# Kernel optimization log

Measured on AMD Instinct MI355X. Metric: run time of the kernel, lower is better.

Reference implementation:

```python
import jax, jax.numpy as jnp
import numpy as np

D_MODEL = 512
NHEAD = 4
HEAD_DIM = D_MODEL // NHEAD


def setup_inputs() -> dict:
    key = jax.random.key(0)
    ks = jax.random.split(key, 12)
    B, S = 2, 4096
    s = 1.0 / np.sqrt(D_MODEL)
    inp = {
        "query": jax.random.normal(ks[0], (B, S, D_MODEL), jnp.float32),
        "key": jax.random.normal(ks[1], (B, S, D_MODEL), jnp.float32),
        "value": jax.random.normal(ks[2], (B, S, D_MODEL), jnp.float32),
        "Wq": jax.random.uniform(ks[3], (D_MODEL, D_MODEL), jnp.float32, -s, s),
        "bq": jax.random.uniform(ks[4], (D_MODEL,), jnp.float32, -s, s),
        "Wk": jax.random.uniform(ks[5], (D_MODEL, D_MODEL), jnp.float32, -s, s),
        "bk": jax.random.uniform(ks[6], (D_MODEL,), jnp.float32, -s, s),
        "Wv": jax.random.uniform(ks[7], (D_MODEL, D_MODEL), jnp.float32, -s, s),
        "bv": jax.random.uniform(ks[8], (D_MODEL,), jnp.float32, -s, s),
        "Wo": jax.random.uniform(ks[9], (D_MODEL, D_MODEL), jnp.float32, -s, s),
        "bo": jax.random.uniform(ks[10], (D_MODEL,), jnp.float32, -s, s),
    }
    return inp


def reference(query, key, value, Wq, bq, Wk, bk, Wv, bv, Wo, bo):
    B, Sq, _ = query.shape
    Sk = key.shape[1]
    # projections (torch Linear: x @ W.T + b); split heads -> [B, H, S, hd]
    def proj(x, W, b, S):
        return (x @ W.T + b).reshape(B, S, NHEAD, HEAD_DIM).transpose(0, 2, 1, 3)
    Q = proj(query, Wq, bq, Sq)
    K = proj(key, Wk, bk, Sk)
    V = proj(value, Wv, bv, Sk)
    scale = 1.0 / np.sqrt(HEAD_DIM).astype(np.float32)
    scores = jnp.einsum("bhqd,bhkd->bhqk", Q, K) * scale  # [B,H,Sq,Sk]
    weights = jax.nn.softmax(scores, axis=-1)
    out = jnp.einsum("bhqk,bhkd->bhqd", weights, V)  # [B,H,Sq,hd]
    out = out.transpose(0, 2, 1, 3).reshape(B, Sq, D_MODEL)
    return out @ Wo.T + bo
```

## Files before the change

kernel.cpp:

```cpp
#include <hip/hip_runtime.h>


#define D_MODEL 512
#define NHEAD 4
#define HD 128
#define S_ 4096

typedef __attribute__((ext_vector_type(8))) short bf16x8;
typedef __attribute__((ext_vector_type(4))) short bf16x4;
typedef __attribute__((ext_vector_type(4))) float f32x4;
typedef __attribute__((ext_vector_type(2))) unsigned uint2v;
typedef __attribute__((ext_vector_type(4))) unsigned uint4v;

#define SCQ (0.08838834764831845f * 1.4426950408889634f)

__device__ __forceinline__ short f2bf(float f) {
    unsigned u = __builtin_bit_cast(unsigned, f);
    u += 0x7fffu + ((u >> 16) & 1u);
    return (short)(u >> 16);
}
__device__ __forceinline__ unsigned pk2bf(float a, float b) {
    unsigned ua = __builtin_bit_cast(unsigned, a);
    ua += 0x7fffu + ((ua >> 16) & 1u);
    unsigned ub = __builtin_bit_cast(unsigned, b);
    ub += 0x7fffu + ((ub >> 16) & 1u);
    return (ua >> 16) | (ub & 0xffff0000u);
}
__device__ __forceinline__ void gl2lds16(const short* g, short* l) {
    __builtin_amdgcn_global_load_lds(
        (const __attribute__((address_space(1))) void*)g,
        (__attribute__((address_space(3))) void*)l, 16, 0, 0);
}

__global__ __launch_bounds__(256) void convert_kernel(
    const float* __restrict__ s0, const float* __restrict__ s1,
    const float* __restrict__ s2, const float* __restrict__ s3,
    const float* __restrict__ s4, const float* __restrict__ s5,
    const float* __restrict__ s6,
    short* __restrict__ d0, short* __restrict__ d1, short* __restrict__ d2,
    short* __restrict__ d3, short* __restrict__ d4, short* __restrict__ d5,
    short* __restrict__ d6)
{
    int seg = blockIdx.y;
    const float* src; short* dst; int n;
    const int NBIG = 2 * S_ * D_MODEL;
    const int NW = D_MODEL * D_MODEL;
    switch (seg) {
        case 0: src = s0; dst = d0; n = NBIG; break;
        case 1: src = s1; dst = d1; n = NBIG; break;
        case 2: src = s2; dst = d2; n = NBIG; break;
        case 3: src = s3; dst = d3; n = NW; break;
        case 4: src = s4; dst = d4; n = NW; break;
        case 5: src = s5; dst = d5; n = NW; break;
        default: src = s6; dst = d6; n = NW; break;
    }
    int idx = (blockIdx.x * 256 + threadIdx.x) * 8;
    if (idx >= n) return;
    float4 a = *(const float4*)(src + idx);
    float4 b = *(const float4*)(src + idx + 4);
    uint4v o;
    o[0] = pk2bf(a.x, a.y); o[1] = pk2bf(a.z, a.w);
    o[2] = pk2bf(b.x, b.y); o[3] = pk2bf(b.z, b.w);
    *(uint4v*)(dst + idx) = o;
}

__global__ __launch_bounds__(256) void qkv_kernel(
    const short* __restrict__ qb, const short* __restrict__ kb,
    const short* __restrict__ vb,
    const short* __restrict__ Wqb, const short* __restrict__ Wkb,
    const short* __restrict__ Wvb,
    const float* __restrict__ bq, const float* __restrict__ bk,
    const float* __restrict__ bv,
    short* __restrict__ Qh, short* __restrict__ Kh, short* __restrict__ VT)
{
    __shared__ short smem[24576];
    int z = blockIdx.z;
    const short* A    = (z == 0) ? qb  : (z == 1) ? kb  : vb;
    const short* W    = (z == 0) ? Wqb : (z == 1) ? Wkb : Wvb;
    const float* bias = (z == 0) ? bq  : (z == 1) ? bk  : bv;
    short* out        = (z == 0) ? Qh  : (z == 1) ? Kh  : VT;
    int vmode = (z == 2);
    float osc = (z == 0) ? SCQ : 1.0f;

    int t = threadIdx.x;
    int wv = t >> 6, ln = t & 63, q4 = ln >> 4, c = ln & 15;
    int m0 = blockIdx.x * 64, n0 = blockIdx.y * 128;
    f32x4 acc[8] = {};

    {
        short* lAd = smem;
        short* lBd = smem + 8192;
        #pragma unroll
        for (int i = 0; i < 2; ++i) {
            int id = i * 256 + t;
            int m = id >> 3, kgp = id & 7;
            gl2lds16(A + (size_t)(m0 + m) * 512 + ((kgp ^ (m & 7)) << 3), &lAd[id * 8]);
        }
        #pragma unroll
        for (int i = 0; i < 4; ++i) {
            int id = i * 256 + t;
            int n = id >> 3, kgp = id & 7;
            gl2lds16(W + (size_t)(n0 + n) * 512 + ((kgp ^ (n & 7)) << 3), &lBd[id * 8]);
        }
    }
    asm volatile("s_waitcnt vmcnt(0)" ::: "memory");
    __builtin_amdgcn_s_barrier();
    __builtin_amdgcn_sched_barrier(0);

    int cur = 0;
    for (int k0 = 0; k0 < 512; k0 += 64) {
        int more = (k0 < 448);
        if (more) {
            short* lAd = smem + (cur ^ 1) * 4096;
            short* lBd = smem + 8192 + (cur ^ 1) * 8192;
            int kn = k0 + 64;
            #pragma unroll
            for (int i = 0; i < 2; ++i) {
                int id = i * 256 + t;
                int m = id >> 3, kgp = id & 7;
                gl2lds16(A + (size_t)(m0 + m) * 512 + kn + ((kgp ^ (m & 7)) << 3), &lAd[id * 8]);
            }
            #pragma unroll
            for (int i = 0; i < 4; ++i) {
                int id = i * 256 + t;
                int n = id >> 3, kgp = id & 7;
                gl2lds16(W + (size_t)(n0 + n) * 512 + kn + ((kgp ^ (n & 7)) << 3), &lBd[id * 8]);
            }
        }
        short* lAc = smem + cur * 4096;
        short* lBc = smem + 8192 + cur * 8192;
        __builtin_amdgcn_s_setprio(1);
        #pragma unroll
        for (int ks = 0; ks < 2; ++ks) {
            int kg = ks * 4 + q4;
            int m = wv * 16 + c;
            bf16x8 af = *(bf16x8*)&lAc[m * 64 + ((kg ^ (m & 7)) << 3)];
            bf16x8 bfr[8];
            #pragma unroll
            for (int nt = 0; nt < 8; ++nt) {
                int n = nt * 16 + c;
                bfr[nt] = *(bf16x8*)&lBc[n * 64 + ((kg ^ (n & 7)) << 3)];
            }
            #pragma unroll
            for (int nt = 0; nt < 8; ++nt)
                acc[nt] = __builtin_amdgcn_mfma_f32_16x16x32_bf16(af, bfr[nt], acc[nt], 0, 0, 0);
        }
        __builtin_amdgcn_s_setprio(0);
        if (more) asm volatile("s_waitcnt vmcnt(0)" ::: "memory");
        __builtin_amdgcn_s_barrier();
        __builtin_amdgcn_sched_barrier(0);
        cur ^= 1;
    }

    if (vmode == 0) {
        const int TS = 136;
        short* lT = smem;
        for (int nt = 0; nt < 8; ++nt) {
            float bv_ = bias[n0 + nt * 16 + c];
            for (int r = 0; r < 4; ++r) {
                int srow = wv * 16 + q4 * 4 + r;
                lT[srow * TS + nt * 16 + c] = f2bf((acc[nt][r] + bv_) * osc);
            }
        }
        __syncthreads();
        int bb = m0 >> 12, sbase = m0 & 4095, h = blockIdx.y;
        for (int i = 0; i < 4; ++i) {
            int id = i * 256 + t;
            int row = id >> 4, g = id & 15;
            bf16x8 vv = *(bf16x8*)&lT[row * TS + g * 8];
            *(bf16x8*)&out[((size_t)((bb * NHEAD + h) * S_ + sbase + row)) * HD + g * 8] = vv;
        }
    } else {
        short* lB0 = smem + 8192;
        for (int nt = 0; nt < 8; ++nt) {
            int d = nt * 16 + c;
            float bv_ = bias[n0 + d];
            uint2v pv;
            pv[0] = pk2bf(acc[nt][0] + bv_, acc[nt][1] + bv_);
            pv[1] = pk2bf(acc[nt][2] + bv_, acc[nt][3] + bv_);
            int gr = wv * 4 + q4;
            *(uint2v*)&lB0[d * 64 + ((gr ^ (d & 15)) << 2)] = pv;
        }
        __syncthreads();
        int bb = m0 >> 12, sbase = m0 & 4095, h = blockIdx.y;
        for (int i = 0; i < 8; ++i) {
            int id = i * 256 + t;
            int d = id >> 4, grl = id & 15;
            bf16x4 v = *(bf16x4*)&lB0[d * 64 + ((grl ^ (d & 15)) << 2)];
            *(bf16x4*)&out[((size_t)((bb * NHEAD + h) * HD + d)) * S_ + sbase + grl * 4] = v;
        }
    }
}

__global__ __launch_bounds__(256) void outproj_kernel(
    const short* __restrict__ A, const short* __restrict__ W,
    const float* __restrict__ bias, float* __restrict__ out)
{
    __shared__ short smem[24576];
    int t = threadIdx.x;
    int wv = t >> 6, ln = t & 63, q4 = ln >> 4, c = ln & 15;
    int m0 = blockIdx.x * 64, n0 = blockIdx.y * 128;
    f32x4 acc[8] = {};

    {
        short* lAd = smem;
        short* lBd = smem + 8192;
        #pragma unroll
        for (int i = 0; i < 2; ++i) {
            int id = i * 256 + t;
            int m = id >> 3, kgp = id & 7;
            gl2lds16(A + (size_t)(m0 + m) * 512 + ((kgp ^ (m & 7)) << 3), &lAd[id * 8]);
        }
        #pragma unroll
        for (int i = 0; i < 4; ++i) {
            int id = i * 256 + t;
            int n = id >> 3, kgp = id & 7;
            gl2lds16(W + (size_t)(n0 + n) * 512 + ((kgp ^ (n & 7)) << 3), &lBd[id * 8]);
        }
    }
    asm volatile("s_waitcnt vmcnt(0)" ::: "memory");
    __builtin_amdgcn_s_barrier();
    __builtin_amdgcn_sched_barrier(0);

    int cur = 0;
    for (int k0 = 0; k0 < 512; k0 += 64) {
        int more = (k0 < 448);
        if (more) {
            short* lAd = smem + (cur ^ 1) * 4096;
            short* lBd = smem + 8192 + (cur ^ 1) * 8192;
            int kn = k0 + 64;
            #pragma unroll
            for (int i = 0; i < 2; ++i) {
                int id = i * 256 + t;
                int m = id >> 3, kgp = id & 7;
                gl2lds16(A + (size_t)(m0 + m) * 512 + kn + ((kgp ^ (m & 7)) << 3), &lAd[id * 8]);
            }
            #pragma unroll
            for (int i = 0; i < 4; ++i) {
                int id = i * 256 + t;
                int n = id >> 3, kgp = id & 7;
                gl2lds16(W + (size_t)(n0 + n) * 512 + kn + ((kgp ^ (n & 7)) << 3), &lBd[id * 8]);
            }
        }
        short* lAc = smem + cur * 4096;
        short* lBc = smem + 8192 + cur * 8192;
        __builtin_amdgcn_s_setprio(1);
        #pragma unroll
        for (int ks = 0; ks < 2; ++ks) {
            int kg = ks * 4 + q4;
            int m = wv * 16 + c;
            bf16x8 af = *(bf16x8*)&lAc[m * 64 + ((kg ^ (m & 7)) << 3)];
            bf16x8 bfr[8];
            #pragma unroll
            for (int nt = 0; nt < 8; ++nt) {
                int n = nt * 16 + c;
                bfr[nt] = *(bf16x8*)&lBc[n * 64 + ((kg ^ (n & 7)) << 3)];
            }
            #pragma unroll
            for (int nt = 0; nt < 8; ++nt)
                acc[nt] = __builtin_amdgcn_mfma_f32_16x16x32_bf16(af, bfr[nt], acc[nt], 0, 0, 0);
        }
        __builtin_amdgcn_s_setprio(0);
        if (more) asm volatile("s_waitcnt vmcnt(0)" ::: "memory");
        __builtin_amdgcn_s_barrier();
        __builtin_amdgcn_sched_barrier(0);
        cur ^= 1;
    }

    for (int nt = 0; nt < 8; ++nt) {
        int col = n0 + nt * 16 + c;
        float bv_ = bias[col];
        for (int r = 0; r < 4; ++r) {
            int mrow = m0 + wv * 16 + q4 * 4 + r;
            out[(size_t)mrow * 512 + col] = acc[nt][r] + bv_;
        }
    }
}

__global__ __launch_bounds__(256, 2) void flash_kernel(
    const short* __restrict__ Qh, const short* __restrict__ Kh,
    const short* __restrict__ VTg, short* __restrict__ AO,
    float* __restrict__ U, float* __restrict__ ML, int nsplit, int kkspan)
{
    __shared__ short lK[2][64 * 128];
    __shared__ short lVT[128 * 64];
    int t = threadIdx.x;
    int wv = t >> 6, ln = t & 63, q4 = ln >> 4, c = ln & 15;
    int bh = blockIdx.x;
    int s0 = blockIdx.y * 128;
    int z = blockIdx.z;
    const size_t base = (size_t)bh * S_ * HD;

    bf16x8 qf[2][4];
    #pragma unroll
    for (int qt = 0; qt < 2; ++qt) {
        int s = s0 + wv * 32 + qt * 16 + c;
        const short* qp = Qh + base + (size_t)s * HD + q4 * 8;
        #pragma unroll
        for (int ks = 0; ks < 4; ++ks)
            qf[qt][ks] = *(const bf16x8*)(qp + ks * 32);
    }

    f32x4 of[8][2] = {};
    float lrun[2] = {};

    int kkbeg = z * kkspan;
    int nt = kkspan >> 6;

    #pragma unroll
    for (int i = 0; i < 4; ++i) {
        int id = i * 256 + t;
        int m = id >> 4, kgp = id & 15;
        gl2lds16(Kh + base + (size_t)(kkbeg + m) * HD + ((kgp ^ (m & 7)) << 3),
                 &lK[0][id * 8]);
    }
    #pragma unroll
    for (int i = 0; i < 4; ++i) {
        int id = i * 256 + t;
        int mv = id >> 3, kgvp = id & 7;
        gl2lds16(VTg + base + (size_t)mv * S_ + kkbeg + ((kgvp ^ (mv & 7)) << 3),
                 &lVT[id * 8]);
    }
    asm volatile("s_waitcnt vmcnt(4)" ::: "memory");
    __builtin_amdgcn_s_barrier();
    __builtin_amdgcn_sched_barrier(0);

    int cur = 0;
    for (int it = 0; it < nt; ++it) {
        int kk0 = kkbeg + it * 64;
        int more = (it + 1 < nt);

        if (more) {
            #pragma unroll
            for (int i = 0; i < 4; ++i) {
                int id = i * 256 + t;
                int m = id >> 4, kgp = id & 15;
                gl2lds16(Kh + base + (size_t)(kk0 + 64 + m) * HD + ((kgp ^ (m & 7)) << 3),
                         &lK[cur ^ 1][id * 8]);
            }
        }

        f32x4 sf[2][4] = {};
        __builtin_amdgcn_s_setprio(1);
        #pragma unroll
        for (int ks = 0; ks < 4; ++ks) {
            int kg = ks * 4 + q4;
            bf16x8 af[4];
            #pragma unroll
            for (int kt = 0; kt < 4; ++kt) {
                int row = kt * 16 + c;
                af[kt] = *(bf16x8*)&lK[cur][row * 128 + ((kg ^ (row & 7)) << 3)];
            }
            #pragma unroll
            for (int qt = 0; qt < 2; ++qt)
                #pragma unroll
                for (int kt = 0; kt < 4; ++kt)
                    sf[qt][kt] = __builtin_amdgcn_mfma_f32_16x16x32_bf16(
                        af[kt], qf[qt][ks], sf[qt][kt], 0, 0, 0);
        }
        __builtin_amdgcn_s_setprio(0);

        bf16x8 bp[2][2];
        #pragma unroll
        for (int qt = 0; qt < 2; ++qt) {
            unsigned dlo[4], dhi[4];
            float lt = 0.f;
            #pragma unroll
            for (int kt = 0; kt < 4; ++kt) {
                float p0 = exp2f(sf[qt][kt][0]);
                float p1 = exp2f(sf[qt][kt][1]);
                float p2 = exp2f(sf[qt][kt][2]);
                float p3 = exp2f(sf[qt][kt][3]);
                lt += (p0 + p1) + (p2 + p3);
                asm("v_cvt_pk_bf16_f32 %0, %1, %2" : "=v"(dlo[kt]) : "v"(p0), "v"(p1));
                asm("v_cvt_pk_bf16_f32 %0, %1, %2" : "=v"(dhi[kt]) : "v"(p2), "v"(p3));
            }
            lrun[qt] += lt;
            #pragma unroll
            for (int ksv = 0; ksv < 2; ++ksv) {
                unsigned x0 = dlo[2 * ksv], y0 = dlo[2 * ksv + 1];
                unsigned x1 = dhi[2 * ksv], y1 = dhi[2 * ksv + 1];
                asm("v_permlane32_swap_b32 %0, %1" : "+v"(x0), "+v"(y0));
                asm("v_permlane16_swap_b32 %0, %1" : "+v"(x0), "+v"(y0));
                asm("v_permlane32_swap_b32 %0, %1" : "+v"(x1), "+v"(y1));
                asm("v_permlane16_swap_b32 %0, %1" : "+v"(x1), "+v"(y1));
                uint4v u; u[0] = x0; u[1] = x1; u[2] = y0; u[3] = y1;
                bp[qt][ksv] = __builtin_bit_cast(bf16x8, u);
            }
        }

        if (more) asm volatile("s_waitcnt vmcnt(4)" ::: "memory");
        else      asm volatile("s_waitcnt vmcnt(0)" ::: "memory");
        __builtin_amdgcn_s_barrier();
        __builtin_amdgcn_sched_barrier(0);

        __builtin_amdgcn_s_setprio(1);
        #pragma unroll
        for (int ksv = 0; ksv < 2; ++ksv) {
            int kg = ksv * 4 + q4;
            bf16x8 av[8];
            #pragma unroll
            for (int dt = 0; dt < 8; ++dt) {
                int row = dt * 16 + c;
                av[dt] = *(bf16x8*)&lVT[row * 64 + ((kg ^ (row & 7)) << 3)];
            }
            #pragma unroll
            for (int qt = 0; qt < 2; ++qt)
                #pragma unroll
                for (int dt = 0; dt < 8; ++dt)
                    of[dt][qt] = __builtin_amdgcn_mfma_f32_16x16x32_bf16(
                        av[dt], bp[qt][ksv], of[dt][qt], 0, 0, 0);
        }
        __builtin_amdgcn_s_setprio(0);

        asm volatile("s_waitcnt vmcnt(0)" ::: "memory");
        __builtin_amdgcn_s_barrier();
        __builtin_amdgcn_sched_barrier(0);

        if (more) {
            #pragma unroll
            for (int i = 0; i < 4; ++i) {
                int id = i * 256 + t;
                int mv = id >> 3, kgvp = id & 7;
                gl2lds16(VTg + base + (size_t)mv * S_ + kk0 + 64 + ((kgvp ^ (mv & 7)) << 3),
                         &lVT[id * 8]);
            }
        }
        cur ^= 1;
    }

    #pragma unroll
    for (int qt = 0; qt < 2; ++qt) {
        lrun[qt] += __shfl_xor(lrun[qt], 16);
        lrun[qt] += __shfl_xor(lrun[qt], 32);
    }

    if (nsplit > 1) {
        #pragma unroll
        for (int qt = 0; qt < 2; ++qt) {
            int s = s0 + wv * 32 + qt * 16 + c;
            size_t rowu = (size_t)(z * 8 + bh) * S_ + s;
            float* up = U + rowu * HD;
            #pragma unroll
            for (int dt = 0; dt < 8; ++dt)
                *(f32x4*)&up[dt * 16 + q4 * 4] = of[dt][qt];
            if (q4 == 0) ML[rowu] = lrun[qt];
        }
    } else {
        int b = bh >> 2, h = bh & 3;
        #pragma unroll
        for (int qt = 0; qt < 2; ++qt) {
            float inv = 1.0f / lrun[qt];
            int s = s0 + wv * 32 + qt * 16 + c;
            short* dst = AO + ((size_t)(b * S_ + s)) * D_MODEL + h * HD;
            #pragma unroll
            for (int dt = 0; dt < 8; ++dt) {
                uint2v ov;
                ov[0] = pk2bf(of[dt][qt][0] * inv, of[dt][qt][1] * inv);
                ov[1] = pk2bf(of[dt][qt][2] * inv, of[dt][qt][3] * inv);
                *(uint2v*)(dst + dt * 16 + q4 * 4) = ov;
            }
        }
    }
}

__global__ __launch_bounds__(256) void combine_kernel(
    const float* __restrict__ U, const float* __restrict__ ML,
    short* __restrict__ AO, int nsplit)
{
    int row = blockIdx.x * 8 + (threadIdx.x >> 5);
    int d4 = (threadIdx.x & 31) * 4;
    const int R = 8 * S_;
    float l = 0.f;
    f32x4 u = {0.f, 0.f, 0.f, 0.f};
    for (int zz = 0; zz < nsplit; ++zz) {
        l += ML[(size_t)zz * R + row];
        f32x4 uz = *(const f32x4*)&U[((size_t)zz * R + row) * HD + d4];
        u += uz;
    }
    float inv = 1.0f / l;
    uint2v o;
    o[0] = pk2bf(u[0] * inv, u[1] * inv);
    o[1] = pk2bf(u[2] * inv, u[3] * inv);
    int bh = row >> 12, s = row & 4095;
    int b = bh >> 2, h = bh & 3;
    *(uint2v*)&AO[((size_t)(b * S_ + s)) * D_MODEL + h * HD + d4] = o;
}

extern "C" void kernel_launch(void* const* d_in, const int* in_sizes, int n_in,
                              void* d_out, int out_size, void* d_ws, size_t ws_size,
                              hipStream_t stream) {
    const float* q  = (const float*)d_in[0];
    const float* k  = (const float*)d_in[1];
    const float* v  = (const float*)d_in[2];
    const float* Wq = (const float*)d_in[3];
    const float* bq = (const float*)d_in[4];
    const float* Wk = (const float*)d_in[5];
    const float* bk = (const float*)d_in[6];
    const float* Wv = (const float*)d_in[7];
    const float* bv = (const float*)d_in[8];
    const float* Wo = (const float*)d_in[9];
    const float* bo = (const float*)d_in[10];

    const size_t HS = (size_t)2 * NHEAD * S_ * HD;
    const size_t NBIG = HS;
    const size_t NW = (size_t)D_MODEL * D_MODEL;
    const size_t R = (size_t)8 * S_;

    char* wsb = (char*)d_ws;
    short* Qh = (short*)wsb;
    short* Kh = Qh + HS;
    short* VT = Kh + HS;
    short* AO = VT + HS;
    char* r2 = wsb + 4 * HS * 2;
    short* qb  = (short*)r2;
    short* kb  = qb + NBIG;
    short* vb  = kb + NBIG;
    short* Wqb = vb + NBIG;
    short* Wkb = Wqb + NW;
    short* Wvb = Wkb + NW;
    float* U   = (float*)r2;

    int nsplit = 1;
    size_t r2sz = 3 * NBIG * 2 + 3 * NW * 2;
    {
        int cand = 2;
        size_t r2c = (size_t)cand * R * HD * 4;
        if (r2c < 3 * NBIG * 2 + 3 * NW * 2) r2c = 3 * NBIG * 2 + 3 * NW * 2;
        size_t need = 4 * HS * 2 + r2c + (size_t)cand * R * 4 + NW * 2;
        if (ws_size >= need) { nsplit = cand; r2sz = r2c; }
    }
    float* ML  = (float*)(r2 + r2sz);
    short* Wob = (short*)((char*)ML + (size_t)nsplit * R * 4);
    int kkspan = S_ / nsplit;

    dim3 blk(256);
    convert_kernel<<<dim3(2048, 7), blk, 0, stream>>>(
        q, k, v, Wq, Wk, Wv, Wo, qb, kb, vb, Wqb, Wkb, Wvb, Wob);
    qkv_kernel<<<dim3(128, 4, 3), blk, 0, stream>>>(
        qb, kb, vb, Wqb, Wkb, Wvb, bq, bk, bv, Qh, Kh, VT);
    flash_kernel<<<dim3(8, 32, nsplit), blk, 0, stream>>>(
        Qh, Kh, VT, AO, U, ML, nsplit, kkspan);
    if (nsplit > 1)
        combine_kernel<<<dim3(S_), blk, 0, stream>>>(U, ML, AO, nsplit);
    outproj_kernel<<<dim3(128, 4), blk, 0, stream>>>(AO, Wob, bo, (float*)d_out);
}
```

Measured before the change: 228.4 us.

## Software-pipeline flash loop: overlap QK of next tile with PV of previous

```diff
diff --git a/kernel.cpp b/kernel.cpp
--- a/kernel.cpp
+++ b/kernel.cpp
@@ -277,13 +277,105 @@
     }
 }
 
+__device__ __forceinline__ void stage_k(const short* __restrict__ Kh, size_t base,
+                                        int kk, short* dst, int t) {
+    #pragma unroll
+    for (int i = 0; i < 4; ++i) {
+        int id = i * 256 + t;
+        int m = id >> 4, kgp = id & 15;
+        gl2lds16(Kh + base + (size_t)(kk + m) * HD + ((kgp ^ (m & 7)) << 3), &dst[id * 8]);
+    }
+}
+__device__ __forceinline__ void stage_vt(const short* __restrict__ VTg, size_t base,
+                                         int kk, short* dst, int t) {
+    #pragma unroll
+    for (int i = 0; i < 4; ++i) {
+        int id = i * 256 + t;
+        int mv = id >> 3, kgvp = id & 7;
+        gl2lds16(VTg + base + (size_t)mv * S_ + kk + ((kgvp ^ (mv & 7)) << 3), &dst[id * 8]);
+    }
+}
+__device__ __forceinline__ void qk_tile(const short* kb, const bf16x8 (&qf)[2][4],
+                                        int q4, int c, f32x4 (&sf)[2][4]) {
+    #pragma unroll
+    for (int ks = 0; ks < 4; ++ks) {
+        int kg = ks * 4 + q4;
+        bf16x8 af[4];
+        #pragma unroll
+        for (int kt = 0; kt < 4; ++kt) {
+            int row = kt * 16 + c;
+            af[kt] = *(bf16x8*)&kb[row * 128 + ((kg ^ (row & 7)) << 3)];
+        }
+        #pragma unroll
+        for (int qt = 0; qt < 2; ++qt)
+            #pragma unroll
+            for (int kt = 0; kt < 4; ++kt)
+                sf[qt][kt] = __builtin_amdgcn_mfma_f32_16x16x32_bf16(
+                    af[kt], qf[qt][ks], sf[qt][kt], 0, 0, 0);
+    }
+}
+__device__ __forceinline__ void pv_tile(const short* vb, const bf16x8 (&bp)[2][2],
+                                        int q4, int c, f32x4 (&of)[8][2]) {
+    #pragma unroll
+    for (int ksv = 0; ksv < 2; ++ksv) {
+        int kg = ksv * 4 + q4;
+        bf16x8 av[8];
+        #pragma unroll
+        for (int dt = 0; dt < 8; ++dt) {
+            int row = dt * 16 + c;
+            av[dt] = *(bf16x8*)&vb[row * 64 + ((kg ^ (row & 7)) << 3)];
+        }
+        #pragma unroll
+        for (int qt = 0; qt < 2; ++qt)
+            #pragma unroll
+            for (int dt = 0; dt < 8; ++dt)
+                of[dt][qt] = __builtin_amdgcn_mfma_f32_16x16x32_bf16(
+                    av[dt], bp[qt][ksv], of[dt][qt], 0, 0, 0);
+    }
+}
+__device__ __forceinline__ void sm_tile(const f32x4 (&sf)[2][4], float (&lrun)[2],
+                                        bf16x8 (&bp)[2][2]) {
+    #pragma unroll
+    for (int qt = 0; qt < 2; ++qt) {
+        unsigned dlo[4], dhi[4];
+        float lt = 0.f;
+        #pragma unroll
+        for (int kt = 0; kt < 4; ++kt) {
+            float p0 = exp2f(sf[qt][kt][0]);
+            float p1 = exp2f(sf[qt][kt][1]);
+            float p2 = exp2f(sf[qt][kt][2]);
+            float p3 = exp2f(sf[qt][kt][3]);
+            lt += (p0 + p1) + (p2 + p3);
+            asm("v_cvt_pk_bf16_f32 %0, %1, %2" : "=v"(dlo[kt]) : "v"(p0), "v"(p1));
+            asm("v_cvt_pk_bf16_f32 %0, %1, %2" : "=v"(dhi[kt]) : "v"(p2), "v"(p3));
+        }
+        lrun[qt] += lt;
+        #pragma unroll
+        for (int ksv = 0; ksv < 2; ++ksv) {
+            unsigned x0 = dlo[2 * ksv], y0 = dlo[2 * ksv + 1];
+            unsigned x1 = dhi[2 * ksv], y1 = dhi[2 * ksv + 1];
+            asm("v_permlane32_swap_b32 %0, %1" : "+v"(x0), "+v"(y0));
+            asm("v_permlane16_swap_b32 %0, %1" : "+v"(x0), "+v"(y0));
+            asm("v_permlane32_swap_b32 %0, %1" : "+v"(x1), "+v"(y1));
+            asm("v_permlane16_swap_b32 %0, %1" : "+v"(x1), "+v"(y1));
+            uint4v u; u[0] = x0; u[1] = x1; u[2] = y0; u[3] = y1;
+            bp[qt][ksv] = __builtin_bit_cast(bf16x8, u);
+        }
+    }
+}
+
+#define FLASH_BAR() do { \
+    asm volatile("s_waitcnt vmcnt(0)" ::: "memory"); \
+    __builtin_amdgcn_s_barrier(); \
+    __builtin_amdgcn_sched_barrier(0); } while (0)
+
 __global__ __launch_bounds__(256, 2) void flash_kernel(
     const short* __restrict__ Qh, const short* __restrict__ Kh,
     const short* __restrict__ VTg, short* __restrict__ AO,
     float* __restrict__ U, float* __restrict__ ML, int nsplit, int kkspan)
 {
     __shared__ short lK[2][64 * 128];
-    __shared__ short lVT[128 * 64];
+    __shared__ short lVT[2][128 * 64];
     int t = threadIdx.x;
     int wv = t >> 6, ln = t & 63, q4 = ln >> 4, c = ln & 15;
     int bh = blockIdx.x;
@@ -303,131 +395,67 @@
 
     f32x4 of[8][2] = {};
     float lrun[2] = {};
+    bf16x8 bpA[2][2], bpB[2][2];
 
     int kkbeg = z * kkspan;
-    int nt = kkspan >> 6;
-
-    #pragma unroll
-    for (int i = 0; i < 4; ++i) {
-        int id = i * 256 + t;
-        int m = id >> 4, kgp = id & 15;
-        gl2lds16(Kh + base + (size_t)(kkbeg + m) * HD + ((kgp ^ (m & 7)) << 3),
-                 &lK[0][id * 8]);
-    }
-    #pragma unroll
-    for (int i = 0; i < 4; ++i) {
-        int id = i * 256 + t;
-        int mv = id >> 3, kgvp = id & 7;
-        gl2lds16(VTg + base + (size_t)mv * S_ + kkbeg + ((kgvp ^ (mv & 7)) << 3),
-                 &lVT[id * 8]);
-    }
-    asm volatile("s_waitcnt vmcnt(4)" ::: "memory");
-    __builtin_amdgcn_s_barrier();
-    __builtin_amdgcn_sched_barrier(0);
-
-    int cur = 0;
-    for (int it = 0; it < nt; ++it) {
-        int kk0 = kkbeg + it * 64;
-        int more = (it + 1 < nt);
-
-        if (more) {
-            #pragma unroll
-            for (int i = 0; i < 4; ++i) {
-                int id = i * 256 + t;
-                int m = id >> 4, kgp = id & 15;
-                gl2lds16(Kh + base + (size_t)(kk0 + 64 + m) * HD + ((kgp ^ (m & 7)) << 3),
-                         &lK[cur ^ 1][id * 8]);
-            }
-        }
-
+    int ntl = kkspan >> 6;
+
+    stage_k(Kh, base, kkbeg, &lK[0][0], t);
+    FLASH_BAR();
+
+    {
+        stage_k(Kh, base, kkbeg + 64, &lK[1][0], t);
+        stage_vt(VTg, base, kkbeg, &lVT[0][0], t);
         f32x4 sf[2][4] = {};
         __builtin_amdgcn_s_setprio(1);
-        #pragma unroll
-        for (int ks = 0; ks < 4; ++ks) {
-            int kg = ks * 4 + q4;
-            bf16x8 af[4];
-            #pragma unroll
-            for (int kt = 0; kt < 4; ++kt) {
-                int row = kt * 16 + c;
-                af[kt] = *(bf16x8*)&lK[cur][row * 128 + ((kg ^ (row & 7)) << 3)];
-            }
-            #pragma unroll
-            for (int qt = 0; qt < 2; ++qt)
-                #pragma unroll
-                for (int kt = 0; kt < 4; ++kt)
-                    sf[qt][kt] = __builtin_amdgcn_mfma_f32_16x16x32_bf16(
-                        af[kt], qf[qt][ks], sf[qt][kt], 0, 0, 0);
-        }
+        qk_tile(&lK[0][0], qf, q4, c, sf);
         __builtin_amdgcn_s_setprio(0);
-
-        bf16x8 bp[2][2];
-        #pragma unroll
-        for (int qt = 0; qt < 2; ++qt) {
-            unsigned dlo[4], dhi[4];
-            float lt = 0.f;
-            #pragma unroll
-            for (int kt = 0; kt < 4; ++kt) {
-                float p0 = exp2f(sf[qt][kt][0]);
-                float p1 = exp2f(sf[qt][kt][1]);
-                float p2 = exp2f(sf[qt][kt][2]);
-                float p3 = exp2f(sf[qt][kt][3]);
-                lt += (p0 + p1) + (p2 + p3);
-                asm("v_cvt_pk_bf16_f32 %0, %1, %2" : "=v"(dlo[kt]) : "v"(p0), "v"(p1));
-                asm("v_cvt_pk_bf16_f32 %0, %1, %2" : "=v"(dhi[kt]) : "v"(p2), "v"(p3));
-            }
-            lrun[qt] += lt;
-            #pragma unroll
-            for (int ksv = 0; ksv < 2; ++ksv) {
-                unsigned x0 = dlo[2 * ksv], y0 = dlo[2 * ksv + 1];
-                unsigned x1 = dhi[2 * ksv], y1 = dhi[2 * ksv + 1];
-                asm("v_permlane32_swap_b32 %0, %1" : "+v"(x0), "+v"(y0));
-                asm("v_permlane16_swap_b32 %0, %1" : "+v"(x0), "+v"(y0));
-                asm("v_permlane32_swap_b32 %0, %1" : "+v"(x1), "+v"(y1));
-                asm("v_permlane16_swap_b32 %0, %1" : "+v"(x1), "+v"(y1));
-                uint4v u; u[0] = x0; u[1] = x1; u[2] = y0; u[3] = y1;
-                bp[qt][ksv] = __builtin_bit_cast(bf16x8, u);
-            }
-        }
-
-        if (more) asm volatile("s_waitcnt vmcnt(4)" ::: "memory");
-        else      asm volatile("s_waitcnt vmcnt(0)" ::: "memory");
-        __builtin_amdgcn_s_barrier();
-        __builtin_amdgcn_sched_barrier(0);
-
+        sm_tile(sf, lrun, bpA);
+        FLASH_BAR();
+    }
+
+    for (int j = 1; j + 1 < ntl; j += 2) {
+        {
+            int kk0 = kkbeg + j * 64;
+            stage_k(Kh, base, kk0 + 64, &lK[0][0], t);
+            stage_vt(VTg, base, kk0, &lVT[1][0], t);
+            f32x4 sf[2][4] = {};
+            __builtin_amdgcn_s_setprio(1);
+            qk_tile(&lK[1][0], qf, q4, c, sf);
+            pv_tile(&lVT[0][0], bpA, q4, c, of);
+            __builtin_amdgcn_s_setprio(0);
+            sm_tile(sf, lrun, bpB);
+            FLASH_BAR();
+        }
+        {
+            int kk0 = kkbeg + (j + 1) * 64;
+            if (j + 2 < ntl) stage_k(Kh, base, kk0 + 64, &lK[1][0], t);
+            stage_vt(VTg, base, kk0, &lVT[0][0], t);
+            f32x4 sf[2][4] = {};
+            __builtin_amdgcn_s_setprio(1);
+            qk_tile(&lK[0][0], qf, q4, c, sf);
+            pv_tile(&lVT[1][0], bpB, q4, c, of);
+            __builtin_amdgcn_s_setprio(0);
+            sm_tile(sf, lrun, bpA);
+            FLASH_BAR();
+        }
+    }
+
+    {
+        int kk0 = kkbeg + (ntl - 1) * 64;
+        stage_vt(VTg, base, kk0, &lVT[1][0], t);
+        f32x4 sf[2][4] = {};
         __builtin_amdgcn_s_setprio(1);
-        #pragma unroll
-        for (int ksv = 0; ksv < 2; ++ksv) {
-            int kg = ksv * 4 + q4;
-            bf16x8 av[8];
-            #pragma unroll
-            for (int dt = 0; dt < 8; ++dt) {
-                int row = dt * 16 + c;
-                av[dt] = *(bf16x8*)&lVT[row * 64 + ((kg ^ (row & 7)) << 3)];
-            }
-            #pragma unroll
-            for (int qt = 0; qt < 2; ++qt)
-                #pragma unroll
-                for (int dt = 0; dt < 8; ++dt)
-                    of[dt][qt] = __builtin_amdgcn_mfma_f32_16x16x32_bf16(
-                        av[dt], bp[qt][ksv], of[dt][qt], 0, 0, 0);
-        }
+        qk_tile(&lK[1][0], qf, q4, c, sf);
+        pv_tile(&lVT[0][0], bpA, q4, c, of);
         __builtin_amdgcn_s_setprio(0);
-
-        asm volatile("s_waitcnt vmcnt(0)" ::: "memory");
-        __builtin_amdgcn_s_barrier();
-        __builtin_amdgcn_sched_barrier(0);
-
-        if (more) {
-            #pragma unroll
-            for (int i = 0; i < 4; ++i) {
-                int id = i * 256 + t;
-                int mv = id >> 3, kgvp = id & 7;
-                gl2lds16(VTg + base + (size_t)mv * S_ + kk0 + 64 + ((kgvp ^ (mv & 7)) << 3),
-                         &lVT[id * 8]);
-            }
-        }
-        cur ^= 1;
-    }
+        sm_tile(sf, lrun, bpB);
+        FLASH_BAR();
+    }
+
+    __builtin_amdgcn_s_setprio(1);
+    pv_tile(&lVT[1][0], bpB, q4, c, of);
+    __builtin_amdgcn_s_setprio(0);
 
     #pragma unroll
     for (int qt = 0; qt < 2; ++qt) {
```

Result: no change. 228.8 us (median of 2 runs) (+0.2%).
